# Kernel tuning notes

Hardware: AMD Instinct MI355X
Metric: run time of the kernel (lower is better)

## Reference

```python
import jax, jax.numpy as jnp
import numpy as np

N = 50000    # nodes
E = 800000   # edges
F = 128      # node_feature_dim
H = 128      # GCN hidden
H2 = 64      # fc1 hidden
T = 8        # num_tactics
G = 64       # graphs in batch


def setup_inputs() -> dict:
    key = jax.random.key(0)
    ks = jax.random.split(key, 12)
    s = 0.05
    return {
        "x": jax.random.normal(ks[0], (N, F), jnp.float32),
        "edge_index": jax.random.randint(ks[1], (2, E), 0, N, dtype=jnp.int32),
        "batch": jnp.sort(jax.random.randint(ks[2], (N,), 0, G, dtype=jnp.int32)),
        "W": jax.random.normal(ks[3], (F, H), jnp.float32) * s,
        "b": jax.random.normal(ks[4], (H,), jnp.float32) * s,
        "fc1_w": jax.random.normal(ks[5], (H, H2), jnp.float32) * s,
        "fc1_b": jax.random.normal(ks[6], (H2,), jnp.float32) * s,
        "actor_w": jax.random.normal(ks[7], (H2, T), jnp.float32) * s,
        "actor_b": jax.random.normal(ks[8], (T,), jnp.float32) * s,
        "critic_w": jax.random.normal(ks[9], (H2, 1), jnp.float32) * s,
        "critic_b": jax.random.normal(ks[10], (1,), jnp.float32) * s,
    }


def _gcn_conv(x, edge_index, W, b):
    # PyG GCNConv: add self-loops, symmetric D^-1/2 (A+I) D^-1/2 normalization,
    # linear transform first, then scatter-add aggregation, then bias.
    n = x.shape[0]
    loops = jnp.arange(n, dtype=edge_index.dtype)
    src = jnp.concatenate([edge_index[0], loops])  # message sources (x_j)
    dst = jnp.concatenate([edge_index[1], loops])  # aggregation targets
    deg = jax.ops.segment_sum(jnp.ones_like(dst, jnp.float32), dst, num_segments=N)
    dinv = deg ** -0.5  # deg >= 1 due to self-loops
    norm = dinv[src] * dinv[dst]                   # [E+N]
    h = x @ W                                      # [N, H]
    msgs = h[src] * norm[:, None]                  # [E+N, H]
    return jax.ops.segment_sum(msgs, dst, num_segments=N) + b


def reference(x, edge_index, batch, W, b, fc1_w, fc1_b, actor_w, actor_b, critic_w, critic_b):
    h = jax.nn.relu(_gcn_conv(x, edge_index, W, b))            # [N, H]
    # global_mean_pool over batch index
    sums = jax.ops.segment_sum(h, batch, num_segments=G)       # [G, H]
    cnts = jax.ops.segment_sum(jnp.ones((h.shape[0],), h.dtype), batch, num_segments=G)
    group_state = sums / jnp.maximum(cnts, 1.0)[:, None]
    z = jax.nn.relu(group_state @ fc1_w + fc1_b)               # [G, H2]
    tactic_probs = jax.nn.softmax(z @ actor_w + actor_b, axis=-1)  # [G, T]
    group_value = z @ critic_w + critic_b                      # [G, 1]
    return tactic_probs, group_value
```

## Files before the change

kernel.cpp:

```cpp
#include <hip/hip_runtime.h>
#include <hip/hip_bf16.h>

#define NN 50000
#define EE 800000
#define FF 128
#define HH 128
#define HID2 64
#define TT 8
#define GG 64
#define NB 196
#define NSB 256
#define EPB (EE / NSB)

__device__ inline unsigned short f2bf(float f) {
    union { float f; unsigned u; } v; v.f = f;
    unsigned r = v.u + 0x7fff + ((v.u >> 16) & 1);
    return (unsigned short)(r >> 16);
}

__global__ __launch_bounds__(256) void kb1(const int* __restrict__ dst,
                                           int* __restrict__ table) {
    __shared__ int cnt[NB];
    int t = threadIdx.x, blk = blockIdx.x;
    for (int i = t; i < NB; i += 256) cnt[i] = 0;
    __syncthreads();
    int e0 = blk * EPB;
    for (int e = e0 + t; e < e0 + EPB; e += 256)
        atomicAdd(&cnt[dst[e] >> 8], 1);
    __syncthreads();
    for (int i = t; i < NB; i += 256) table[blk * NB + i] = cnt[i];
}

__global__ __launch_bounds__(256) void kb2(int* __restrict__ table,
                                           int* __restrict__ bbase) {
    __shared__ int s[256];
    int b = threadIdx.x;
    int tot = 0;
    if (b < NB)
        for (int blk = 0; blk < NSB; blk++) tot += table[blk * NB + b];
    s[b] = (b < NB) ? tot : 0;
    __syncthreads();
    for (int off = 1; off < 256; off <<= 1) {
        int a = s[b];
        int w = (b >= off) ? s[b - off] : 0;
        __syncthreads();
        s[b] = a + w;
        __syncthreads();
    }
    int base = (b == 0) ? 0 : s[b - 1];
    if (b < NB) {
        bbase[b] = base;
        int run = base;
        for (int blk = 0; blk < NSB; blk++) {
            int v = table[blk * NB + b];
            table[blk * NB + b] = run;
            run += v;
        }
    }
    if (b == 0) bbase[NB] = EE;
}

__global__ __launch_bounds__(256) void kb3(const int* __restrict__ src,
                                           const int* __restrict__ dst,
                                           const int* __restrict__ table,
                                           unsigned* __restrict__ etmp) {
    __shared__ int ofs[NB];
    __shared__ int cur[NB];
    int t = threadIdx.x, blk = blockIdx.x;
    for (int i = t; i < NB; i += 256) { ofs[i] = table[blk * NB + i]; cur[i] = 0; }
    __syncthreads();
    int e0 = blk * EPB;
    for (int e = e0 + t; e < e0 + EPB; e += 256) {
        int d = dst[e];
        int b = d >> 8;
        int r = atomicAdd(&cur[b], 1);
        etmp[ofs[b] + r] = ((unsigned)d << 16) | (unsigned)src[e];
    }
}

__global__ __launch_bounds__(256) void k_csr(const unsigned* __restrict__ etmp,
                                             const int* __restrict__ bbase,
                                             int* __restrict__ row_ptr,
                                             float* __restrict__ dinv,
                                             int* __restrict__ srcs) {
    __shared__ int s[256];
    __shared__ int cur[256];
    int t = threadIdx.x, b = blockIdx.x;
    s[t] = 0;
    __syncthreads();
    int e0 = bbase[b], e1 = bbase[b + 1];
    for (int e = e0 + t; e < e1; e += 256)
        atomicAdd(&s[(etmp[e] >> 16) & 255], 1);
    __syncthreads();
    int v = s[t];
    for (int off = 1; off < 256; off <<= 1) {
        int a = s[t];
        int w = (t >= off) ? s[t - off] : 0;
        __syncthreads();
        s[t] = a + w;
        __syncthreads();
    }
    int excl = s[t] - v + e0;
    int node = b * 256 + t;
    if (node < NN) {
        row_ptr[node] = excl;
        dinv[node] = rsqrtf((float)(v + 1));
    }
    if (b == NB - 1 && t == 0) row_ptr[NN] = EE;
    cur[t] = excl;
    __syncthreads();
    for (int e = e0 + t; e < e1; e += 256) {
        unsigned u = etmp[e];
        int slot = atomicAdd(&cur[(u >> 16) & 255], 1);
        srcs[slot] = (int)(u & 0xffffu);
    }
}

__global__ __launch_bounds__(256) void k_gemm(const float* __restrict__ x,
                                              const float* __restrict__ W,
                                              const float* __restrict__ dinv,
                                              unsigned* __restrict__ hs) {
    __shared__ float xs[64 * 36];
    __shared__ float ws[32 * 132];
    int tid = threadIdx.x;
    int tx = tid & 15, ty = tid >> 4;
    int r0 = blockIdx.x * 64;
    float acc[4][8];
#pragma unroll
    for (int r = 0; r < 4; r++)
#pragma unroll
        for (int c = 0; c < 8; c++) acc[r][c] = 0.f;

    for (int k0 = 0; k0 < 128; k0 += 32) {
        {
            int row = tid >> 2, q = tid & 3;
            int gr = r0 + row;
            float4 a0 = {0, 0, 0, 0}, a1 = {0, 0, 0, 0};
            if (gr < NN) {
                const float4* p = (const float4*)(x + (size_t)gr * 128 + k0 + q * 8);
                a0 = p[0]; a1 = p[1];
            }
            float* dp = &xs[row * 36 + q * 8];
            ((float4*)dp)[0] = a0; ((float4*)dp)[1] = a1;
        }
        {
            int kr = tid >> 3, q = tid & 7;
            const float4* p = (const float4*)(W + (size_t)(k0 + kr) * 128 + q * 16);
            float4 b0 = p[0], b1 = p[1], b2 = p[2], b3 = p[3];
            float* dp = &ws[kr * 132 + q * 16];
            ((float4*)dp)[0] = b0; ((float4*)dp)[1] = b1;
            ((float4*)dp)[2] = b2; ((float4*)dp)[3] = b3;
        }
        __syncthreads();
#pragma unroll
        for (int kk = 0; kk < 32; kk++) {
            float a[4];
#pragma unroll
            for (int r = 0; r < 4; r++) a[r] = xs[(ty * 4 + r) * 36 + kk];
            float4 b0 = *(const float4*)&ws[kk * 132 + tx * 8];
            float4 b1 = *(const float4*)&ws[kk * 132 + tx * 8 + 4];
            float bv[8] = {b0.x, b0.y, b0.z, b0.w, b1.x, b1.y, b1.z, b1.w};
#pragma unroll
            for (int r = 0; r < 4; r++)
#pragma unroll
                for (int c = 0; c < 8; c++)
                    acc[r][c] = fmaf(a[r], bv[c], acc[r][c]);
        }
        __syncthreads();
    }
#pragma unroll
    for (int r = 0; r < 4; r++) {
        int gr = r0 + ty * 4 + r;
        if (gr < NN) {
            float di = dinv[gr];
            unsigned p0 = f2bf(acc[r][0] * di) | ((unsigned)f2bf(acc[r][1] * di) << 16);
            unsigned p1 = f2bf(acc[r][2] * di) | ((unsigned)f2bf(acc[r][3] * di) << 16);
            unsigned p2 = f2bf(acc[r][4] * di) | ((unsigned)f2bf(acc[r][5] * di) << 16);
            unsigned p3 = f2bf(acc[r][6] * di) | ((unsigned)f2bf(acc[r][7] * di) << 16);
            uint4 o = {p0, p1, p2, p3};
            *(uint4*)(hs + (size_t)gr * 64 + tx * 4) = o;
        }
    }
}

__global__ __launch_bounds__(256) void k_aggr(const uint4* __restrict__ hs4,
                                              const int* __restrict__ row_ptr,
                                              const int* __restrict__ srcs,
                                              const float* __restrict__ dinv,
                                              const float* __restrict__ bias,
                                              const int* __restrict__ batch,
                                              float* __restrict__ gsum) {
    __shared__ float gacc[GG * 128];
    int tid = threadIdx.x;
    int qid = tid >> 4, sub = tid & 15;
    int i_base = blockIdx.x * 32;
    int g_first = batch[i_base];
    int last = i_base + 31; if (last >= NN) last = NN - 1;
    int gspan = batch[last] - g_first + 1;
    for (int idx = tid; idx < gspan * 128; idx += 256) gacc[idx] = 0.f;
    __syncthreads();

    const float4* b4 = (const float4*)(bias + sub * 8);
    float4 bb0 = b4[0], bb1 = b4[1];

    float racc[8];
#pragma unroll
    for (int j = 0; j < 8; j++) racc[j] = 0.f;
    int cur_lg = -1;

    for (int n = 0; n < 2; n++) {
        int i = i_base + qid * 2 + n;
        if (i >= NN) break;
        int lg = batch[i] - g_first;
        if (lg != cur_lg) {
            if (cur_lg >= 0) {
                float* gp = &gacc[cur_lg * 128 + sub * 8];
#pragma unroll
                for (int j = 0; j < 8; j++) atomicAdd(&gp[j], racc[j]);
#pragma unroll
                for (int j = 0; j < 8; j++) racc[j] = 0.f;
            }
            cur_lg = lg;
        }
        float di = dinv[i];
        uint4 su = hs4[(size_t)i * 16 + sub];
        float a0 = __uint_as_float(su.x << 16);
        float a1 = __uint_as_float(su.x & 0xffff0000u);
        float a2 = __uint_as_float(su.y << 16);
        float a3 = __uint_as_float(su.y & 0xffff0000u);
        float a4 = __uint_as_float(su.z << 16);
        float a5 = __uint_as_float(su.z & 0xffff0000u);
        float a6 = __uint_as_float(su.w << 16);
        float a7 = __uint_as_float(su.w & 0xffff0000u);
        int e = row_ptr[i], e1 = row_ptr[i + 1];
        for (; e + 3 < e1; e += 4) {
            int s0 = srcs[e], s1 = srcs[e + 1], s2 = srcs[e + 2], s3 = srcs[e + 3];
            uint4 u0 = hs4[(size_t)s0 * 16 + sub];
            uint4 u1 = hs4[(size_t)s1 * 16 + sub];
            uint4 u2 = hs4[(size_t)s2 * 16 + sub];
            uint4 u3 = hs4[(size_t)s3 * 16 + sub];
            a0 += __uint_as_float(u0.x << 16); a1 += __uint_as_float(u0.x & 0xffff0000u);
            a2 += __uint_as_float(u0.y << 16); a3 += __uint_as_float(u0.y & 0xffff0000u);
            a4 += __uint_as_float(u0.z << 16); a5 += __uint_as_float(u0.z & 0xffff0000u);
            a6 += __uint_as_float(u0.w << 16); a7 += __uint_as_float(u0.w & 0xffff0000u);
            a0 += __uint_as_float(u1.x << 16); a1 += __uint_as_float(u1.x & 0xffff0000u);
            a2 += __uint_as_float(u1.y << 16); a3 += __uint_as_float(u1.y & 0xffff0000u);
            a4 += __uint_as_float(u1.z << 16); a5 += __uint_as_float(u1.z & 0xffff0000u);
            a6 += __uint_as_float(u1.w << 16); a7 += __uint_as_float(u1.w & 0xffff0000u);
            a0 += __uint_as_float(u2.x << 16); a1 += __uint_as_float(u2.x & 0xffff0000u);
            a2 += __uint_as_float(u2.y << 16); a3 += __uint_as_float(u2.y & 0xffff0000u);
            a4 += __uint_as_float(u2.z << 16); a5 += __uint_as_float(u2.z & 0xffff0000u);
            a6 += __uint_as_float(u2.w << 16); a7 += __uint_as_float(u2.w & 0xffff0000u);
            a0 += __uint_as_float(u3.x << 16); a1 += __uint_as_float(u3.x & 0xffff0000u);
            a2 += __uint_as_float(u3.y << 16); a3 += __uint_as_float(u3.y & 0xffff0000u);
            a4 += __uint_as_float(u3.z << 16); a5 += __uint_as_float(u3.z & 0xffff0000u);
            a6 += __uint_as_float(u3.w << 16); a7 += __uint_as_float(u3.w & 0xffff0000u);
        }
        for (; e < e1; ++e) {
            uint4 u0 = hs4[(size_t)srcs[e] * 16 + sub];
            a0 += __uint_as_float(u0.x << 16); a1 += __uint_as_float(u0.x & 0xffff0000u);
            a2 += __uint_as_float(u0.y << 16); a3 += __uint_as_float(u0.y & 0xffff0000u);
            a4 += __uint_as_float(u0.z << 16); a5 += __uint_as_float(u0.z & 0xffff0000u);
            a6 += __uint_as_float(u0.w << 16); a7 += __uint_as_float(u0.w & 0xffff0000u);
        }
        racc[0] += fmaxf(fmaf(a0, di, bb0.x), 0.f);
        racc[1] += fmaxf(fmaf(a1, di, bb0.y), 0.f);
        racc[2] += fmaxf(fmaf(a2, di, bb0.z), 0.f);
        racc[3] += fmaxf(fmaf(a3, di, bb0.w), 0.f);
        racc[4] += fmaxf(fmaf(a4, di, bb1.x), 0.f);
        racc[5] += fmaxf(fmaf(a5, di, bb1.y), 0.f);
        racc[6] += fmaxf(fmaf(a6, di, bb1.z), 0.f);
        racc[7] += fmaxf(fmaf(a7, di, bb1.w), 0.f);
    }
    if (cur_lg >= 0) {
        float* gp = &gacc[cur_lg * 128 + sub * 8];
#pragma unroll
        for (int j = 0; j < 8; j++) atomicAdd(&gp[j], racc[j]);
    }
    __syncthreads();
    for (int idx = tid; idx < gspan * 128; idx += 256) {
        float v = gacc[idx];
        if (v != 0.f)
            atomicAdd(&gsum[(g_first + (idx >> 7)) * 128 + (idx & 127)], v);
    }
}

__device__ inline int lbound(const int* __restrict__ a, int n, int key) {
    int lo = 0, hi = n;
    while (lo < hi) {
        int mid = (lo + hi) >> 1;
        if (a[mid] < key) lo = mid + 1;
        else hi = mid;
    }
    return lo;
}

__global__ __launch_bounds__(64) void k_head(const float* __restrict__ gsum,
                                             const int* __restrict__ batch,
                                             const float* __restrict__ fc1_w,
                                             const float* __restrict__ fc1_b,
                                             const float* __restrict__ actor_w,
                                             const float* __restrict__ actor_b,
                                             const float* __restrict__ critic_w,
                                             const float* __restrict__ critic_b,
                                             float* __restrict__ out) {
    __shared__ float gs[128];
    __shared__ float zs[64];
    __shared__ float ls[8], es[8];
    int g = blockIdx.x, t = threadIdx.x;
    int lo = lbound(batch, NN, g), hi = lbound(batch, NN, g + 1);
    float invc = 1.f / fmaxf((float)(hi - lo), 1.f);
    gs[t] = gsum[g * 128 + t] * invc;
    gs[t + 64] = gsum[g * 128 + 64 + t] * invc;
    __syncthreads();
    float z = fc1_b[t];
    for (int k = 0; k < 128; k++) z = fmaf(gs[k], fc1_w[k * 64 + t], z);
    zs[t] = fmaxf(z, 0.f);
    __syncthreads();
    if (t < 8) {
        float l = actor_b[t];
        for (int k = 0; k < 64; k++) l = fmaf(zs[k], actor_w[k * 8 + t], l);
        ls[t] = l;
    }
    __syncthreads();
    if (t < 8) {
        float m = ls[0];
#pragma unroll
        for (int j = 1; j < 8; j++) m = fmaxf(m, ls[j]);
        es[t] = expf(ls[t] - m);
    }
    __syncthreads();
    if (t < 8) {
        float ssum = 0.f;
#pragma unroll
        for (int j = 0; j < 8; j++) ssum += es[j];
        out[g * 8 + t] = es[t] / ssum;
    }
    if (t == 32) {
        float v = critic_b[0];
        for (int k = 0; k < 64; k++) v = fmaf(zs[k], critic_w[k], v);
        out[GG * TT + g] = v;
    }
}

extern "C" void kernel_launch(void* const* d_in, const int* in_sizes, int n_in,
                              void* d_out, int out_size, void* d_ws, size_t ws_size,
                              hipStream_t stream) {
    const float* x        = (const float*)d_in[0];
    const int*   ei       = (const int*)d_in[1];
    const int*   batch    = (const int*)d_in[2];
    const float* W        = (const float*)d_in[3];
    const float* b        = (const float*)d_in[4];
    const float* fc1_w    = (const float*)d_in[5];
    const float* fc1_b    = (const float*)d_in[6];
    const float* actor_w  = (const float*)d_in[7];
    const float* actor_b  = (const float*)d_in[8];
    const float* critic_w = (const float*)d_in[9];
    const float* critic_b = (const float*)d_in[10];
    float* out = (float*)d_out;

    char* ws = (char*)d_ws;
    size_t off = 0;
    unsigned* hs     = (unsigned*)(ws + off); off += (size_t)NN * 64 * 4;
    float* dinv      = (float*)(ws + off);    off += (size_t)NN * 4;
    int*   row_ptr   = (int*)(ws + off);      off += (size_t)(NN + 1) * 4 + 12;
    int*   srcs      = (int*)(ws + off);      off += (size_t)EE * 4;
    unsigned* etmp   = (unsigned*)(ws + off); off += (size_t)EE * 4;
    int*   table     = (int*)(ws + off);      off += (size_t)NSB * NB * 4;
    int*   bbase     = (int*)(ws + off);      off += (size_t)(NB + 1) * 4;
    float* gsum      = (float*)(ws + off);    off += (size_t)GG * HH * 4;

    hipMemsetAsync(gsum, 0, (size_t)GG * HH * 4, stream);

    const int* src = ei;
    const int* dst = ei + EE;

    kb1<<<NSB, 256, 0, stream>>>(dst, table);
    kb2<<<1, 256, 0, stream>>>(table, bbase);
    kb3<<<NSB, 256, 0, stream>>>(src, dst, table, etmp);
    k_csr<<<NB, 256, 0, stream>>>(etmp, bbase, row_ptr, dinv, srcs);
    k_gemm<<<(NN + 63) / 64, 256, 0, stream>>>(x, W, dinv, hs);
    k_aggr<<<(NN + 31) / 32, 256, 0, stream>>>((const uint4*)hs, row_ptr, srcs,
                                               dinv, b, batch, gsum);
    k_head<<<GG, 64, 0, stream>>>(gsum, batch, fc1_w, fc1_b, actor_w, actor_b,
                                  critic_w, critic_b, out);
}
```

Measured before the change: 221.2 us.

## Split bf16 hidden features into four column slabs for cache-friendly aggregation

The GEMM now writes the bf16 hidden matrix as four column-quarter slabs, each holding 32 features per node in contiguous 64-byte rows. The aggregation kernel runs four times as many blocks, and each block gathers only one slab. Each slab is about 3.2 MB, so the random neighbor gathers have a much smaller working set that can stay cache-resident. In exchange, the CSR index arrays (row_ptr, srcs) are read four times, and the pooling shared-memory accumulation falls back to global atomics when a 64-node block spans more than 16 graphs.

New measurement: 240.7 us. +8.8%, slower.

```diff
diff --git a/kernel.cpp b/kernel.cpp
--- a/kernel.cpp
+++ b/kernel.cpp
@@ -11,6 +11,8 @@
 #define NB 196
 #define NSB 256
 #define EPB (EE / NSB)
+#define QBLK 782
+#define SLAB ((size_t)NN * 4)
 
 __device__ inline unsigned short f2bf(float f) {
     union { float f; unsigned u; } v; v.f = f;
@@ -119,7 +121,7 @@
 __global__ __launch_bounds__(256) void k_gemm(const float* __restrict__ x,
                                               const float* __restrict__ W,
                                               const float* __restrict__ dinv,
-                                              unsigned* __restrict__ hs) {
+                                              uint4* __restrict__ hsq4) {
     __shared__ float xs[64 * 36];
     __shared__ float ws[32 * 132];
     int tid = threadIdx.x;
@@ -168,6 +170,8 @@
         }
         __syncthreads();
     }
+    int q = tx >> 2, j = tx & 3;
+    uint4* slab = hsq4 + (size_t)q * SLAB;
 #pragma unroll
     for (int r = 0; r < 4; r++) {
         int gr = r0 + ty * 4 + r;
@@ -178,52 +182,35 @@
             unsigned p2 = f2bf(acc[r][4] * di) | ((unsigned)f2bf(acc[r][5] * di) << 16);
             unsigned p3 = f2bf(acc[r][6] * di) | ((unsigned)f2bf(acc[r][7] * di) << 16);
             uint4 o = {p0, p1, p2, p3};
-            *(uint4*)(hs + (size_t)gr * 64 + tx * 4) = o;
-        }
-    }
-}
-
-__global__ __launch_bounds__(256) void k_aggr(const uint4* __restrict__ hs4,
+            slab[(size_t)gr * 4 + j] = o;
+        }
+    }
+}
+
+__global__ __launch_bounds__(256) void k_aggr(const uint4* __restrict__ hsq4,
                                               const int* __restrict__ row_ptr,
                                               const int* __restrict__ srcs,
                                               const float* __restrict__ dinv,
                                               const float* __restrict__ bias,
                                               const int* __restrict__ batch,
                                               float* __restrict__ gsum) {
-    __shared__ float gacc[GG * 128];
-    int tid = threadIdx.x;
-    int qid = tid >> 4, sub = tid & 15;
-    int i_base = blockIdx.x * 32;
-    int g_first = batch[i_base];
-    int last = i_base + 31; if (last >= NN) last = NN - 1;
-    int gspan = batch[last] - g_first + 1;
-    for (int idx = tid; idx < gspan * 128; idx += 256) gacc[idx] = 0.f;
-    __syncthreads();
-
-    const float4* b4 = (const float4*)(bias + sub * 8);
-    float4 bb0 = b4[0], bb1 = b4[1];
-
-    float racc[8];
-#pragma unroll
-    for (int j = 0; j < 8; j++) racc[j] = 0.f;
-    int cur_lg = -1;
-
-    for (int n = 0; n < 2; n++) {
-        int i = i_base + qid * 2 + n;
-        if (i >= NN) break;
-        int lg = batch[i] - g_first;
-        if (lg != cur_lg) {
-            if (cur_lg >= 0) {
-                float* gp = &gacc[cur_lg * 128 + sub * 8];
-#pragma unroll
-                for (int j = 0; j < 8; j++) atomicAdd(&gp[j], racc[j]);
-#pragma unroll
-                for (int j = 0; j < 8; j++) racc[j] = 0.f;
-            }
-            cur_lg = lg;
-        }
-        float di = dinv[i];
-        uint4 su = hs4[(size_t)i * 16 + sub];
+    __shared__ float gacc[16 * 32];
+    int t = threadIdx.x;
+    int q = blockIdx.x / QBLK, nb = blockIdx.x % QBLK;
+    int base = nb * 64;
+    int node = base + (t >> 2);
+    int j = t & 3;
+    int lastn = base + 63; if (lastn >= NN) lastn = NN - 1;
+    int g_first = batch[base];
+    int gspan = batch[lastn] - g_first + 1;
+    int slots = (gspan < 16) ? gspan : 16;
+    for (int idx = t; idx < slots * 32; idx += 256) gacc[idx] = 0.f;
+    __syncthreads();
+
+    const uint4* slab = hsq4 + (size_t)q * SLAB;
+    if (node < NN) {
+        float di = dinv[node];
+        uint4 su = slab[(size_t)node * 4 + j];
         float a0 = __uint_as_float(su.x << 16);
         float a1 = __uint_as_float(su.x & 0xffff0000u);
         float a2 = __uint_as_float(su.y << 16);
@@ -232,13 +219,13 @@
         float a5 = __uint_as_float(su.z & 0xffff0000u);
         float a6 = __uint_as_float(su.w << 16);
         float a7 = __uint_as_float(su.w & 0xffff0000u);
-        int e = row_ptr[i], e1 = row_ptr[i + 1];
+        int e = row_ptr[node], e1 = row_ptr[node + 1];
         for (; e + 3 < e1; e += 4) {
             int s0 = srcs[e], s1 = srcs[e + 1], s2 = srcs[e + 2], s3 = srcs[e + 3];
-            uint4 u0 = hs4[(size_t)s0 * 16 + sub];
-            uint4 u1 = hs4[(size_t)s1 * 16 + sub];
-            uint4 u2 = hs4[(size_t)s2 * 16 + sub];
-            uint4 u3 = hs4[(size_t)s3 * 16 + sub];
+            uint4 u0 = slab[(size_t)s0 * 4 + j];
+            uint4 u1 = slab[(size_t)s1 * 4 + j];
+            uint4 u2 = slab[(size_t)s2 * 4 + j];
+            uint4 u3 = slab[(size_t)s3 * 4 + j];
             a0 += __uint_as_float(u0.x << 16); a1 += __uint_as_float(u0.x & 0xffff0000u);
             a2 += __uint_as_float(u0.y << 16); a3 += __uint_as_float(u0.y & 0xffff0000u);
             a4 += __uint_as_float(u0.z << 16); a5 += __uint_as_float(u0.z & 0xffff0000u);
@@ -257,31 +244,44 @@
             a6 += __uint_as_float(u3.w << 16); a7 += __uint_as_float(u3.w & 0xffff0000u);
         }
         for (; e < e1; ++e) {
-            uint4 u0 = hs4[(size_t)srcs[e] * 16 + sub];
+            uint4 u0 = slab[(size_t)srcs[e] * 4 + j];
             a0 += __uint_as_float(u0.x << 16); a1 += __uint_as_float(u0.x & 0xffff0000u);
             a2 += __uint_as_float(u0.y << 16); a3 += __uint_as_float(u0.y & 0xffff0000u);
             a4 += __uint_as_float(u0.z << 16); a5 += __uint_as_float(u0.z & 0xffff0000u);
             a6 += __uint_as_float(u0.w << 16); a7 += __uint_as_float(u0.w & 0xffff0000u);
         }
-        racc[0] += fmaxf(fmaf(a0, di, bb0.x), 0.f);
-        racc[1] += fmaxf(fmaf(a1, di, bb0.y), 0.f);
-        racc[2] += fmaxf(fmaf(a2, di, bb0.z), 0.f);
-        racc[3] += fmaxf(fmaf(a3, di, bb0.w), 0.f);
-        racc[4] += fmaxf(fmaf(a4, di, bb1.x), 0.f);
-        racc[5] += fmaxf(fmaf(a5, di, bb1.y), 0.f);
-        racc[6] += fmaxf(fmaf(a6, di, bb1.z), 0.f);
-        racc[7] += fmaxf(fmaf(a7, di, bb1.w), 0.f);
-    }
-    if (cur_lg >= 0) {
-        float* gp = &gacc[cur_lg * 128 + sub * 8];
-#pragma unroll
-        for (int j = 0; j < 8; j++) atomicAdd(&gp[j], racc[j]);
-    }
-    __syncthreads();
-    for (int idx = tid; idx < gspan * 128; idx += 256) {
-        float v = gacc[idx];
-        if (v != 0.f)
-            atomicAdd(&gsum[(g_first + (idx >> 7)) * 128 + (idx & 127)], v);
+        const float4* b4 = (const float4*)(bias + q * 32 + j * 8);
+        float4 bb0 = b4[0], bb1 = b4[1];
+        float r0 = fmaxf(fmaf(a0, di, bb0.x), 0.f);
+        float r1 = fmaxf(fmaf(a1, di, bb0.y), 0.f);
+        float r2 = fmaxf(fmaf(a2, di, bb0.z), 0.f);
+        float r3 = fmaxf(fmaf(a3, di, bb0.w), 0.f);
+        float r4 = fmaxf(fmaf(a4, di, bb1.x), 0.f);
+        float r5 = fmaxf(fmaf(a5, di, bb1.y), 0.f);
+        float r6 = fmaxf(fmaf(a6, di, bb1.z), 0.f);
+        float r7 = fmaxf(fmaf(a7, di, bb1.w), 0.f);
+        int g = batch[node];
+        if (gspan <= 16) {
+            float* gp = &gacc[(g - g_first) * 32 + j * 8];
+            atomicAdd(&gp[0], r0); atomicAdd(&gp[1], r1);
+            atomicAdd(&gp[2], r2); atomicAdd(&gp[3], r3);
+            atomicAdd(&gp[4], r4); atomicAdd(&gp[5], r5);
+            atomicAdd(&gp[6], r6); atomicAdd(&gp[7], r7);
+        } else {
+            float* gp = &gsum[g * 128 + q * 32 + j * 8];
+            atomicAdd(&gp[0], r0); atomicAdd(&gp[1], r1);
+            atomicAdd(&gp[2], r2); atomicAdd(&gp[3], r3);
+            atomicAdd(&gp[4], r4); atomicAdd(&gp[5], r5);
+            atomicAdd(&gp[6], r6); atomicAdd(&gp[7], r7);
+        }
+    }
+    __syncthreads();
+    if (gspan <= 16) {
+        for (int idx = t; idx < slots * 32; idx += 256) {
+            float v = gacc[idx];
+            if (v != 0.f)
+                atomicAdd(&gsum[(g_first + (idx >> 5)) * 128 + q * 32 + (idx & 31)], v);
+        }
     }
 }
 
@@ -361,7 +361,7 @@
 
     char* ws = (char*)d_ws;
     size_t off = 0;
-    unsigned* hs     = (unsigned*)(ws + off); off += (size_t)NN * 64 * 4;
+    uint4* hsq4      = (uint4*)(ws + off);    off += (size_t)NN * 64 * 4;
     float* dinv      = (float*)(ws + off);    off += (size_t)NN * 4;
     int*   row_ptr   = (int*)(ws + off);      off += (size_t)(NN + 1) * 4 + 12;
     int*   srcs      = (int*)(ws + off);      off += (size_t)EE * 4;
@@ -379,9 +379,8 @@
     kb2<<<1, 256, 0, stream>>>(table, bbase);
     kb3<<<NSB, 256, 0, stream>>>(src, dst, table, etmp);
     k_csr<<<NB, 256, 0, stream>>>(etmp, bbase, row_ptr, dinv, srcs);
-    k_gemm<<<(NN + 63) / 64, 256, 0, stream>>>(x, W, dinv, hs);
-    k_aggr<<<(NN + 31) / 32, 256, 0, stream>>>((const uint4*)hs, row_ptr, srcs,
-                                               dinv, b, batch, gsum);
+    k_gemm<<<(NN + 63) / 64, 256, 0, stream>>>(x, W, dinv, hsq4);
+    k_aggr<<<4 * QBLK, 256, 0, stream>>>(hsq4, row_ptr, srcs, dinv, b, batch, gsum);
     k_head<<<GG, 64, 0, stream>>>(gsum, batch, fc1_w, fc1_b, actor_w, actor_b,
                                   critic_w, critic_b, out);
 }
```
